# Performance work log

Measured on AMD Instinct MI355X. Metric: run time of the kernel, lower is better.

The kernel has to match this reference:

```python
import jax, jax.numpy as jnp
import numpy as np

B, TXT_T, MEL_T, N_MEL = 8, 200, 800, 80
PAD_MAG = 1.0e12


def setup_inputs() -> dict:
    key = jax.random.key(0)
    k1, k2, k3, k4 = jax.random.split(key, 4)
    mu_logvar = jax.random.normal(k1, (B, TXT_T, 2 * N_MEL), dtype=jnp.float32)
    melspec = jax.random.normal(k2, (B, N_MEL, MEL_T), dtype=jnp.float32)
    # lengths are 1-based (indexed as length-1), keep them in [T//2, T]
    text_lengths = jax.random.randint(k3, (B,), TXT_T // 2, TXT_T + 1)
    mel_lengths = jax.random.randint(k4, (B,), MEL_T // 2, MEL_T + 1)
    return {
        "mu_logvar": mu_logvar,
        "melspec": melspec,
        "text_lengths": text_lengths,
        "mel_lengths": mel_lengths,
    }


def _log_prob_matrix(mu_logvar, melspec):
    # melspec: [B, n_mel, mel_T] -> x: [B, 1, mel_T, n_mel]
    x = jnp.transpose(melspec, (0, 2, 1))[:, None, :, :]
    mu = mu_logvar[:, :, :N_MEL][:, :, None, :]       # [B, txt_T, 1, n_mel]
    logvar = mu_logvar[:, :, N_MEL:][:, :, None, :]   # [B, txt_T, 1, n_mel]
    # -0.5 * mean_over_mel( (x-mu)^2 / exp(logvar) + logvar )
    sq = (x - mu) ** 2
    return (-0.5 * (sq * jnp.exp(-logvar) + logvar)).mean(axis=3)  # [B, txt_T, mel_T]


def reference(mu_logvar, melspec, text_lengths, mel_lengths):
    lp = _log_prob_matrix(mu_logvar, melspec)  # [B, txt_T, mel_T]

    # log_alpha column carry, with a leading pad row (index 0 stays -PAD_MAG)
    init = jnp.full((B, TXT_T + 1), -PAD_MAG, dtype=lp.dtype)
    init = init.at[:, 1].set(lp[:, 0, 0])

    def step(a, lp_t):  # a: [B, txt_T+1], lp_t: [B, txt_T]
        # logsumexp over {stay, advance}; original adds 1e-7 to prev values
        new_rows = jnp.logaddexp(a[:, 1:] + 1e-7, a[:, :-1] + 1e-7) + lp_t
        a = a.at[:, 1:].set(new_rows)
        return a, new_rows

    lp_rest = jnp.moveaxis(lp[:, :, 1:], 2, 0)  # [mel_T-1, B, txt_T]
    _, cols = jax.lax.scan(step, init, lp_rest)  # cols: [mel_T-1, B, txt_T]

    log_alpha = jnp.concatenate(
        [init[:, 1:, None], jnp.moveaxis(cols, 0, 2)], axis=2
    )  # [B, txt_T, mel_T]

    b = jnp.arange(B)
    alpha_last = log_alpha[b, text_lengths - 1, mel_lengths - 1]
    alpha_last = alpha_last / mel_lengths.astype(alpha_last.dtype)
    mdn_loss = -alpha_last.mean()
    return mdn_loss, lp
```

## Files before the change

### kernel.cpp

```cpp
#include <hip/hip_runtime.h>
#include <math.h>

#define BB 8
#define TXT_T 200
#define MEL_T 800
#define N_MEL 80
#define PAD_MAG 1.0e12f
#define LPT_STRIDE 200

__device__ __forceinline__ float laddexp(float a, float b) {
    float m = fmaxf(a, b);
    float d = fabsf(a - b);
    float e = __expf(-d);
    return m + 1e-7f + 0.69314718055994530942f * __log2f(1.0f + e);
}

__global__ void __launch_bounds__(256) lp_kernel(
        const float* __restrict__ mu_logvar,
        const float* __restrict__ melspec,
        float* __restrict__ out_lp,
        float* __restrict__ lpT) {
    const int bt = blockIdx.x;
    const int b  = bt / TXT_T;
    const int t  = bt % TXT_T;
    const int tid = threadIdx.x;

    __shared__ float s_mu[N_MEL];
    __shared__ float s_ev[N_MEL];
    __shared__ float s_lv[N_MEL];
    __shared__ float s_sumlv;

    if (tid < N_MEL) {
        float mu = mu_logvar[(size_t)bt * (2 * N_MEL) + tid];
        float lv = mu_logvar[(size_t)bt * (2 * N_MEL) + N_MEL + tid];
        s_mu[tid] = mu;
        s_ev[tid] = __expf(-lv);
        s_lv[tid] = lv;
    }
    __syncthreads();
    if (tid == 0) {
        float s = 0.f;
        #pragma unroll
        for (int n = 0; n < N_MEL; ++n) s += s_lv[n];
        s_sumlv = s;
    }
    __syncthreads();

    if (tid < MEL_T / 4) {
        const float4* ms4 = (const float4*)(melspec + (size_t)b * N_MEL * MEL_T);
        float ax = 0.f, ay = 0.f, az = 0.f, aw = 0.f;
        #pragma unroll 8
        for (int n = 0; n < N_MEL; ++n) {
            float4 x = ms4[(size_t)n * (MEL_T / 4) + tid];
            float mu = s_mu[n];
            float ev = s_ev[n];
            float d0 = x.x - mu; ax += d0 * d0 * ev;
            float d1 = x.y - mu; ay += d1 * d1 * ev;
            float d2 = x.z - mu; az += d2 * d2 * ev;
            float d3 = x.w - mu; aw += d3 * d3 * ev;
        }
        const float c = -0.5f / (float)N_MEL;
        float slv = s_sumlv;
        float l0 = c * (ax + slv);
        float l1 = c * (ay + slv);
        float l2 = c * (az + slv);
        float l3 = c * (aw + slv);

        size_t ob = (size_t)bt * MEL_T + tid * 4;
        out_lp[ob + 0] = l0;
        out_lp[ob + 1] = l1;
        out_lp[ob + 2] = l2;
        out_lp[ob + 3] = l3;

        int m0 = tid * 4;
        size_t tb = ((size_t)b * MEL_T + m0) * LPT_STRIDE + t;
        lpT[tb + 0 * LPT_STRIDE] = l0;
        lpT[tb + 1 * LPT_STRIDE] = l1;
        lpT[tb + 2 * LPT_STRIDE] = l2;
        lpT[tb + 3 * LPT_STRIDE] = l3;
    }
}

#define PF 8

#define STEP(VK, TT) do {                                                     \
    float4 lp_ = VK;                                                          \
    int row_ = (TT) + PF;                                                     \
    row_ = row_ > (MEL_T - 1) ? (MEL_T - 1) : row_;                           \
    VK = *(const float4*)(base + (size_t)row_ * LPT_STRIDE + jc);             \
    float left_ = __shfl_up(r3, 1);                                           \
    if (lane == 0) left_ = -PAD_MAG;             \
    float n0_ = laddexp(r0, left_) + lp_.x;                                   \
    float n1_ = laddexp(r1, r0)    + lp_.y;                                   \
    float n2_ = laddexp(r2, r1)    + lp_.z;                                   \
    float n3_ = laddexp(r3, r2)    + lp_.w;                                   \
    r0 = n0_; r1 = n1_; r2 = n2_; r3 = n3_;                                   \
    if ((TT) == melL1 && lane == alane) {                                     \
        float v_ = (acomp == 0) ? r0 : (acomp == 1) ? r1                      \
                 : (acomp == 2) ? r2 : r3;                                    \
        alpha_out[b] = v_ * inv_mel;                                          \
    }                                                                         \
} while (0)

__global__ void __launch_bounds__(64) scan_kernel(
        const float* __restrict__ lpT,
        const int* __restrict__ text_lengths,
        const int* __restrict__ mel_lengths,
        float* __restrict__ alpha_out) {
    const int b = blockIdx.x;
    const int lane = threadIdx.x;
    const float* base = lpT + (size_t)b * MEL_T * LPT_STRIDE;

    int j0 = lane * 4;
    int jc = j0 > (TXT_T - 4) ? (TXT_T - 4) : j0;

    const int melL1 = mel_lengths[b] - 1;
    const int txtL1 = text_lengths[b] - 1;
    const float inv_mel = 1.0f / (float)(melL1 + 1);
    const int alane = txtL1 >> 2;
    const int acomp = txtL1 & 3;

    float r0 = -PAD_MAG, r1 = -PAD_MAG, r2 = -PAD_MAG, r3 = -PAD_MAG;
    float lp00 = base[0];
    if (lane == 0) r0 = lp00;

    if (melL1 == 0 && lane == alane) {
        float v = (acomp == 0) ? r0 : (acomp == 1) ? r1 : (acomp == 2) ? r2 : r3;
        alpha_out[b] = v * inv_mel;
    }

    float4 v0 = *(const float4*)(base + (size_t)1 * LPT_STRIDE + jc);
    float4 v1 = *(const float4*)(base + (size_t)2 * LPT_STRIDE + jc);
    float4 v2 = *(const float4*)(base + (size_t)3 * LPT_STRIDE + jc);
    float4 v3 = *(const float4*)(base + (size_t)4 * LPT_STRIDE + jc);
    float4 v4 = *(const float4*)(base + (size_t)5 * LPT_STRIDE + jc);
    float4 v5 = *(const float4*)(base + (size_t)6 * LPT_STRIDE + jc);
    float4 v6 = *(const float4*)(base + (size_t)7 * LPT_STRIDE + jc);
    float4 v7 = *(const float4*)(base + (size_t)8 * LPT_STRIDE + jc);

    for (int t = 1; t < MEL_T; t += PF) {
        STEP(v0, t + 0);
        STEP(v1, t + 1);
        STEP(v2, t + 2);
        STEP(v3, t + 3);
        STEP(v4, t + 4);
        STEP(v5, t + 5);
        STEP(v6, t + 6);
        STEP(v7, t + 7);
    }
}

__global__ void finish_kernel(const float* __restrict__ alpha,
                              float* __restrict__ out) {
    float s = 0.f;
    #pragma unroll
    for (int b = 0; b < BB; ++b) s += alpha[b];
    out[0] = -(s / (float)BB);
}

extern "C" void kernel_launch(void* const* d_in, const int* in_sizes, int n_in,
                              void* d_out, int out_size, void* d_ws, size_t ws_size,
                              hipStream_t stream) {
    const float* mu_logvar    = (const float*)d_in[0];
    const float* melspec      = (const float*)d_in[1];
    const int*   text_lengths = (const int*)d_in[2];
    const int*   mel_lengths  = (const int*)d_in[3];
    float* out = (float*)d_out;

    float* alpha = (float*)d_ws;
    float* lpT   = (float*)d_ws + 16;

    lp_kernel<<<BB * TXT_T, 256, 0, stream>>>(mu_logvar, melspec, out + 1, lpT);
    scan_kernel<<<BB, 64, 0, stream>>>(lpT, text_lengths, mel_lengths, alpha);
    finish_kernel<<<1, 1, 0, stream>>>(alpha, out);
}
```

Baseline: 158.2 us.

## Run scan in log2 domain with 8 rows per lane and two batches per wave

The lp kernel now writes the transposed log-prob matrix pre-scaled by log2(e) with the 1e-7 epsilon folded in, so the scan recursion works in base 2 using raw hardware exp2/log2 and fewer multiplies. Each lane now owns 8 text rows instead of 4, so one 64-lane wave handles two batches in halves of 32 lanes, and the scan launches 4 blocks instead of 8. The change shortens the serial per-step instruction chain, but each lane does twice as many dependent logaddexp ops per step, so per-step latency on the critical path may grow.

```diff
diff --git a/kernel.cpp b/kernel.cpp
--- a/kernel.cpp
+++ b/kernel.cpp
@@ -5,14 +5,24 @@
 #define TXT_T 200
 #define MEL_T 800
 #define N_MEL 80
-#define PAD_MAG 1.0e12f
 #define LPT_STRIDE 200
+#define LOG2E 1.44269504088896340736f
+#define LN2   0.69314718055994530942f
+#define EPS2  (1e-7f * LOG2E)
+#define NPAD  -1.0e12f
 
-__device__ __forceinline__ float laddexp(float a, float b) {
-    float m = fmaxf(a, b);
-    float d = fabsf(a - b);
-    float e = __expf(-d);
-    return m + 1e-7f + 0.69314718055994530942f * __log2f(1.0f + e);
+__device__ __forceinline__ float exp2_hw(float x) {
+#if __has_builtin(__builtin_amdgcn_exp2f)
+    return __builtin_amdgcn_exp2f(x);
+#else
+    return __expf(LN2 * x);
+#endif
+}
+
+__device__ __forceinline__ float lse2(float A, float B) {
+    float m = fmaxf(A, B);
+    float e = exp2_hw(-fabsf(A - B));
+    return m + __log2f(1.0f + e);
 }
 
 __global__ void __launch_bounds__(256) lp_kernel(
@@ -74,31 +84,43 @@
 
         int m0 = tid * 4;
         size_t tb = ((size_t)b * MEL_T + m0) * LPT_STRIDE + t;
-        lpT[tb + 0 * LPT_STRIDE] = l0;
-        lpT[tb + 1 * LPT_STRIDE] = l1;
-        lpT[tb + 2 * LPT_STRIDE] = l2;
-        lpT[tb + 3 * LPT_STRIDE] = l3;
+        lpT[tb + 0 * LPT_STRIDE] = l0 * LOG2E + EPS2;
+        lpT[tb + 1 * LPT_STRIDE] = l1 * LOG2E + EPS2;
+        lpT[tb + 2 * LPT_STRIDE] = l2 * LOG2E + EPS2;
+        lpT[tb + 3 * LPT_STRIDE] = l3 * LOG2E + EPS2;
     }
 }
 
 #define PF 8
+#define LD(row)  (*(const float4*)(base + (size_t)(row) * LPT_STRIDE))
+#define LD2(row) (*(const float4*)(base + (size_t)(row) * LPT_STRIDE + 4))
 
-#define STEP(VK, TT) do {                                                     \
-    float4 lp_ = VK;                                                          \
+#define STEP(AK, BK, TT) do {                                                 \
+    float4 lpA_ = AK; float4 lpB_ = BK;                                       \
     int row_ = (TT) + PF;                                                     \
     row_ = row_ > (MEL_T - 1) ? (MEL_T - 1) : row_;                           \
-    VK = *(const float4*)(base + (size_t)row_ * LPT_STRIDE + jc);             \
-    float left_ = __shfl_up(r3, 1);                                           \
-    if (lane == 0) left_ = -PAD_MAG;             \
-    float n0_ = laddexp(r0, left_) + lp_.x;                                   \
-    float n1_ = laddexp(r1, r0)    + lp_.y;                                   \
-    float n2_ = laddexp(r2, r1)    + lp_.z;                                   \
-    float n3_ = laddexp(r3, r2)    + lp_.w;                                   \
-    r0 = n0_; r1 = n1_; r2 = n2_; r3 = n3_;                                   \
-    if ((TT) == melL1 && lane == alane) {                                     \
-        float v_ = (acomp == 0) ? r0 : (acomp == 1) ? r1                      \
-                 : (acomp == 2) ? r2 : r3;                                    \
-        alpha_out[b] = v_ * inv_mel;                                          \
+    AK = LD(row_); BK = LD2(row_);                                            \
+    float left_ = __shfl_up(r7, 1);                                           \
+    if (li == 0) left_ = NPAD;     \
+    float n0_ = lse2(r0, left_) + lpA_.x;                                     \
+    float n1_ = lse2(r1, r0)    + lpA_.y;                                     \
+    float n2_ = lse2(r2, r1)    + lpA_.z;                                     \
+    float n3_ = lse2(r3, r2)    + lpA_.w;                                     \
+    float n4_ = lse2(r4, r3)    + lpB_.x;                                     \
+    float n5_ = lse2(r5, r4)    + lpB_.y;                                     \
+    float n6_ = lse2(r6, r5)    + lpB_.z;                                     \
+    float n7_ = lse2(r7, r6)    + lpB_.w;                                     \
+    r0=n0_; r1=n1_; r2=n2_; r3=n3_; r4=n4_; r5=n5_; r6=n6_; r7=n7_;           \
+    if ((TT) == myMel) {      \
+        float v_ = r0;                                                        \
+        if (acomp == 1) v_ = r1;                                              \
+        if (acomp == 2) v_ = r2;                                              \
+        if (acomp == 3) v_ = r3;                                              \
+        if (acomp == 4) v_ = r4;                                              \
+        if (acomp == 5) v_ = r5;                                              \
+        if (acomp == 6) v_ = r6;                                              \
+        if (acomp == 7) v_ = r7;                                              \
+        alpha_out[batch] = v_ * scale;                                        \
     }                                                                         \
 } while (0)
 
@@ -107,46 +129,43 @@
         const int* __restrict__ text_lengths,
         const int* __restrict__ mel_lengths,
         float* __restrict__ alpha_out) {
-    const int b = blockIdx.x;
     const int lane = threadIdx.x;
-    const float* base = lpT + (size_t)b * MEL_T * LPT_STRIDE;
+    const int half = lane >> 5;
+    const int li   = lane & 31;
+    const int batch = blockIdx.x * 2 + half;
+    int jl = li * 8;
+    jl = jl > (TXT_T - 8) ? (TXT_T - 8) : jl;
 
-    int j0 = lane * 4;
-    int jc = j0 > (TXT_T - 4) ? (TXT_T - 4) : j0;
+    const int melL1 = mel_lengths[batch] - 1;
+    const int txtL1 = text_lengths[batch] - 1;
+    const float scale = LN2 / (float)(melL1 + 1);
+    const int acomp = txtL1 & 7;
+    const int myMel = (li == (txtL1 >> 3)) ? melL1 : -1;
 
-    const int melL1 = mel_lengths[b] - 1;
-    const int txtL1 = text_lengths[b] - 1;
-    const float inv_mel = 1.0f / (float)(melL1 + 1);
-    const int alane = txtL1 >> 2;
-    const int acomp = txtL1 & 3;
+    const float* base = lpT + (size_t)batch * MEL_T * LPT_STRIDE + jl;
 
-    float r0 = -PAD_MAG, r1 = -PAD_MAG, r2 = -PAD_MAG, r3 = -PAD_MAG;
-    float lp00 = base[0];
-    if (lane == 0) r0 = lp00;
+    float4 i0 = LD(0);
+    float r0 = (li == 0) ? (i0.x - EPS2) : NPAD;
+    float r1 = NPAD, r2 = NPAD, r3 = NPAD, r4 = NPAD, r5 = NPAD, r6 = NPAD, r7 = NPAD;
 
-    if (melL1 == 0 && lane == alane) {
-        float v = (acomp == 0) ? r0 : (acomp == 1) ? r1 : (acomp == 2) ? r2 : r3;
-        alpha_out[b] = v * inv_mel;
-    }
-
-    float4 v0 = *(const float4*)(base + (size_t)1 * LPT_STRIDE + jc);
-    float4 v1 = *(const float4*)(base + (size_t)2 * LPT_STRIDE + jc);
-    float4 v2 = *(const float4*)(base + (size_t)3 * LPT_STRIDE + jc);
-    float4 v3 = *(const float4*)(base + (size_t)4 * LPT_STRIDE + jc);
-    float4 v4 = *(const float4*)(base + (size_t)5 * LPT_STRIDE + jc);
-    float4 v5 = *(const float4*)(base + (size_t)6 * LPT_STRIDE + jc);
-    float4 v6 = *(const float4*)(base + (size_t)7 * LPT_STRIDE + jc);
-    float4 v7 = *(const float4*)(base + (size_t)8 * LPT_STRIDE + jc);
+    float4 a0 = LD(1), b0 = LD2(1);
+    float4 a1 = LD(2), b1 = LD2(2);
+    float4 a2 = LD(3), b2 = LD2(3);
+    float4 a3 = LD(4), b3 = LD2(4);
+    float4 a4 = LD(5), b4 = LD2(5);
+    float4 a5 = LD(6), b5 = LD2(6);
+    float4 a6 = LD(7), b6 = LD2(7);
+    float4 a7 = LD(8), b7 = LD2(8);
 
     for (int t = 1; t < MEL_T; t += PF) {
-        STEP(v0, t + 0);
-        STEP(v1, t + 1);
-        STEP(v2, t + 2);
-        STEP(v3, t + 3);
-        STEP(v4, t + 4);
-        STEP(v5, t + 5);
-        STEP(v6, t + 6);
-        STEP(v7, t + 7);
+        STEP(a0, b0, t + 0);
+        STEP(a1, b1, t + 1);
+        STEP(a2, b2, t + 2);
+        STEP(a3, b3, t + 3);
+        STEP(a4, b4, t + 4);
+        STEP(a5, b5, t + 5);
+        STEP(a6, b6, t + 6);
+        STEP(a7, b7, t + 7);
     }
 }
 
@@ -171,6 +190,6 @@
     float* lpT   = (float*)d_ws + 16;
 
     lp_kernel<<<BB * TXT_T, 256, 0, stream>>>(mu_logvar, melspec, out + 1, lpT);
-    scan_kernel<<<BB, 64, 0, stream>>>(lpT, text_lengths, mel_lengths, alpha);
+    scan_kernel<<<BB / 2, 64, 0, stream>>>(lpT, text_lengths, mel_lengths, alpha);
     finish_kernel<<<1, 1, 0, stream>>>(alpha, out);
 }
```

After: 201.6 us. 1.27x slower.
